# Kernel optimization log

Measured on AMD Instinct MI355X. Metric: run time of the kernel, lower is better.

The kernel has to match this reference:

```python
import jax, jax.numpy as jnp
import numpy as np
import math

B, H, S, D = 4, 16, 2048, 128

def setup_inputs() -> dict:
    key = jax.random.key(0)
    kq, kk, kv = jax.random.split(key, 3)
    Q = jax.random.normal(kq, (B, H, S, D), dtype=jnp.float32)
    K = jax.random.normal(kk, (B, H, S, D), dtype=jnp.float32)
    V = jax.random.normal(kv, (B, H, S, D), dtype=jnp.float32)
    return {"Q": Q, "K": K, "V": V}

def reference(Q, K, V):
    # scores: [B, H, S, S]
    scale = 1.0 / math.sqrt(Q.shape[-1])
    scores = jnp.einsum('bhqd,bhkd->bhqk', Q, K) * scale
    attn = jax.nn.softmax(scores, axis=-1)
    return jnp.einsum('bhqk,bhkd->bhqd', attn, V)
```

## Files before the change

### kernel.cpp

```cpp
#include <hip/hip_runtime.h>
#include <stdint.h>

#define BATCH 4
#define HEADS 16
#define SEQ 2048
#define DIM 128

constexpr int QBLK  = 128;
constexpr int KVB   = 64;
constexpr int NKT   = SEQ / KVB;
constexpr int TILEB = KVB * DIM * 2;
constexpr int NBH   = BATCH * HEADS;

constexpr int K0OFF = 0;
constexpr int K1OFF = 16384;
constexpr int V0OFF = 32768;
constexpr int V1OFF = 49152;

typedef __bf16 bf16x8 __attribute__((ext_vector_type(8)));
typedef float  f32x4  __attribute__((ext_vector_type(4)));
typedef float  f32x16 __attribute__((ext_vector_type(16)));
typedef unsigned int uint32;

typedef const __attribute__((address_space(1))) void* gas_t;
typedef __attribute__((address_space(3))) void* las_t;

__device__ __forceinline__ uint32 packbf2(float a, float b) {
  union { __bf16 h[2]; uint32 u; } c;
  c.h[0] = (__bf16)a; c.h[1] = (__bf16)b;
  return c.u;
}

__global__ __launch_bounds__(256)
void prepass(const float* __restrict__ Kg, const float* __restrict__ Vg,
             char* __restrict__ Kws, char* __restrict__ Vws)
{
  __shared__ __bf16 sVt[DIM * 72];
  const int tile = blockIdx.x;
  const int tid  = threadIdx.x;
  const float* Ksrc = Kg + (size_t)tile * KVB * DIM;
  const float* Vsrc = Vg + (size_t)tile * KVB * DIM;
  char* kdst = Kws + (size_t)tile * TILEB;
  char* vdst = Vws + (size_t)tile * TILEB;

#pragma unroll
  for (int c = 0; c < 4; ++c) {
    const int flat8 = (c * 256 + tid) * 8;
    const int kv = flat8 >> 7, d0 = flat8 & 127;
    union { float4 f; float a[4]; } x0, x1;
    x0.f = *(const float4*)(Ksrc + flat8);
    x1.f = *(const float4*)(Ksrc + flat8 + 4);
    bf16x8 kx;
#pragma unroll
    for (int j = 0; j < 4; ++j) { kx[j] = (__bf16)x0.a[j]; kx[4 + j] = (__bf16)x1.a[j]; }
    *(bf16x8*)(kdst + kv * 256 + ((2 * d0) ^ ((kv & 15) << 4))) = kx;

    union { float4 f; float a[4]; } v0, v1;
    v0.f = *(const float4*)(Vsrc + flat8);
    v1.f = *(const float4*)(Vsrc + flat8 + 4);
#pragma unroll
    for (int j = 0; j < 8; ++j) {
      const int d = d0 + j;
      const float vv = (j < 4) ? v0.a[j] : v1.a[j - 4];
      sVt[d * 72 + (kv ^ (((d >> 3) & 7) << 3))] = (__bf16)vv;
    }
  }
  __syncthreads();
#pragma unroll
  for (int c = 0; c < 4; ++c) {
    const int flat8 = (c * 256 + tid) * 8;
    const int d = flat8 >> 6, kv0 = flat8 & 63;
    bf16x8 row = *(const bf16x8*)(&sVt[d * 72 + (kv0 ^ (((d >> 3) & 7) << 3))]);
    *(bf16x8*)(vdst + (d & 63) * 256 +
               ((((d >> 6) << 7) | (2 * kv0)) ^ (((d & 63) & 15) << 4))) = row;
  }
}


#define QK_BODY(KOFF)                                                            \
  {                                                                              \
    s0 = (f32x16)0.0f; s1 = (f32x16)0.0f;                                        \
    __builtin_amdgcn_s_setprio(1);                                               \
    _Pragma("unroll")                                                            \
    for (int k = 0; k < 8; ++k) {                                                \
      bf16x8 kf0 = *(const bf16x8*)(smem + (KOFF) + akv[k]);                     \
      bf16x8 kf1 = *(const bf16x8*)(smem + (KOFF) + 8192 + akv[k]);              \
      s0 = __builtin_amdgcn_mfma_f32_32x32x16_bf16(kf0, qf[k], s0, 0, 0, 0);     \
      s1 = __builtin_amdgcn_mfma_f32_32x32x16_bf16(kf1, qf[k], s1, 0, 0, 0);     \
    }                                                                            \
    __builtin_amdgcn_s_setprio(0);                                               \
  }

#define PV_BODY(VOFF, PB)                                                        \
  {                                                                              \
    __builtin_amdgcn_s_setprio(1);                                               \
    _Pragma("unroll")                                                            \
    for (int td = 0; td < 4; ++td) {                                             \
      _Pragma("unroll")                                                          \
      for (int k = 0; k < 4; ++k) {                                              \
        const int ab = (td >> 1) ? avh[k] : avv[k];                              \
        bf16x8 vf = *(const bf16x8*)(smem + (VOFF) + ab + (td & 1) * 8192);      \
        oacc[td] = __builtin_amdgcn_mfma_f32_32x32x16_bf16(vf, PB[k], oacc[td], 0, 0, 0); \
      }                                                                          \
    }                                                                            \
    __builtin_amdgcn_s_setprio(0);                                               \
  }

#define EXP_BODY(PB)                                                             \
  {                                                                              \
    uint32 pk[2][8];                                                             \
    float rs = 0.f;                                                              \
    _Pragma("unroll")                                                            \
    for (int i = 0; i < 8; ++i) {                                                \
      float a0 = __builtin_amdgcn_exp2f(s0[2*i]);                                \
      float a1 = __builtin_amdgcn_exp2f(s0[2*i+1]);                              \
      float b0 = __builtin_amdgcn_exp2f(s1[2*i]);                                \
      float b1 = __builtin_amdgcn_exp2f(s1[2*i+1]);                              \
      rs += (a0 + a1) + (b0 + b1);                                               \
      pk[0][i] = packbf2(a0, a1);                                                \
      pk[1][i] = packbf2(b0, b1);                                                \
    }                                                                            \
    lrp += rs;                                                                   \
    _Pragma("unroll")                                                            \
    for (int k4 = 0; k4 < 4; ++k4) {                                             \
      const int T = k4 >> 1, a4 = (k4 & 1) * 4;                                  \
      auto r0 = __builtin_amdgcn_permlane32_swap((int)pk[T][a4+0], (int)pk[T][a4+2], false, false); \
      auto r1 = __builtin_amdgcn_permlane32_swap((int)pk[T][a4+1], (int)pk[T][a4+3], false, false); \
      union { uint32 u[4]; bf16x8 v; } w;                                        \
      w.u[0] = (uint32)r0[0]; w.u[1] = (uint32)r1[0];                            \
      w.u[2] = (uint32)r0[1]; w.u[3] = (uint32)r1[1];                            \
      PB[k4] = w.v;                                                              \
    }                                                                            \
  }

#define STAGE_K(DST, kt)                                                         \
  do {                                                                           \
    const char* p_ = Kt + (size_t)(kt) * TILEB;                                  \
    _Pragma("unroll")                                                            \
    for (int c_ = 0; c_ < 4; ++c_) {                                             \
      const int od_ = c_ * 4096 + wid * 1024;                                    \
      __builtin_amdgcn_global_load_lds((gas_t)(p_ + od_ + lane * 16),            \
                                       (las_t)(smem + (DST) + od_), 16, 0, 0);   \
    }                                                                            \
  } while (0)

#define STAGE_V(DST, kt)                                                         \
  do {                                                                           \
    const char* p_ = Vt + (size_t)(kt) * TILEB;                                  \
    _Pragma("unroll")                                                            \
    for (int c_ = 0; c_ < 4; ++c_) {                                             \
      const int od_ = c_ * 4096 + wid * 1024;                                    \
      __builtin_amdgcn_global_load_lds((gas_t)(p_ + od_ + lane * 16),            \
                                       (las_t)(smem + (DST) + od_), 16, 0, 0);   \
    }                                                                            \
  } while (0)

__global__ __launch_bounds__(256, 2)
void attn_fwd(const float* __restrict__ Qg, float* __restrict__ Og,
              const char* __restrict__ Kws, const char* __restrict__ Vws)
{
  __shared__ __align__(16) char smem[65536];

  const int tid  = threadIdx.x;
  const int lane = tid & 63;
  const int wid  = tid >> 6;
  const int l    = lane & 31;
  const int hi   = lane >> 5;

  const int bid = blockIdx.x;
  const int swz = ((bid & 7) << 7) + (bid >> 3);
  const int bh  = swz >> 4;
  const int qb  = swz & 15;

  const float* Qb = Qg + (size_t)bh * SEQ * DIM;
  float*       Ob = Og + (size_t)bh * SEQ * DIM;
  const char*  Kt = Kws + (size_t)bh * NKT * TILEB;
  const char*  Vt = Vws + (size_t)bh * NKT * TILEB;

  const int q0 = qb * QBLK + wid * 32;

  int akv[8], avv[4], avh[4];
#pragma unroll
  for (int k = 0; k < 8; ++k)
    akv[k] = l * 256 + ((k * 32 + hi * 16) ^ ((l & 15) << 4));
#pragma unroll
  for (int k = 0; k < 4; ++k) {
    avv[k] = l * 256 + ((k * 32 + hi * 16) ^ ((l & 15) << 4));
    avh[k] = avv[k] ^ 128;
  }

  STAGE_K(K0OFF, 0);

  const float qscale = 0.08838834764831845f * 1.4426950408889634f;
  bf16x8 qf[8];
  {
    const float* qrow = Qb + (size_t)(q0 + l) * DIM;
#pragma unroll
    for (int k = 0; k < 8; ++k) {
      const int d0 = k * 16 + hi * 8;
      union { float4 f; float a[4]; } x0, x1;
      x0.f = *(const float4*)(qrow + d0);
      x1.f = *(const float4*)(qrow + d0 + 4);
      bf16x8 f;
#pragma unroll
      for (int j = 0; j < 4; ++j) {
        f[j]     = (__bf16)(x0.a[j] * qscale);
        f[4 + j] = (__bf16)(x1.a[j] * qscale);
      }
      qf[k] = f;
    }
  }

  float lrp = 0.f;
  f32x16 s0, s1;
  bf16x8 pbA[4], pbB[4];
  f32x16 oacc[4];
#pragma unroll
  for (int t = 0; t < 4; ++t) oacc[t] = (f32x16)0.0f;

  __syncthreads();

  STAGE_K(K1OFF, 1);
  STAGE_V(V0OFF, 0);
  QK_BODY(K0OFF);
  EXP_BODY(pbA);
  __syncthreads();

#pragma unroll 1
  for (int t = 1; t <= NKT - 3; t += 2) {
    STAGE_K(K0OFF, t + 1);
    STAGE_V(V1OFF, t);
    QK_BODY(K1OFF);
    PV_BODY(V0OFF, pbA);
    EXP_BODY(pbB);
    __syncthreads();

    STAGE_K(K1OFF, t + 2);
    STAGE_V(V0OFF, t + 1);
    QK_BODY(K0OFF);
    PV_BODY(V1OFF, pbB);
    EXP_BODY(pbA);
    __syncthreads();
  }

  STAGE_V(V1OFF, NKT - 1);
  QK_BODY(K1OFF);
  PV_BODY(V0OFF, pbA);
  EXP_BODY(pbB);
  __syncthreads();
  PV_BODY(V1OFF, pbB);

  const float lrow = lrp + __shfl_xor(lrp, 32, 64);
  const float inv = 1.0f / lrow;
  float* sO = (float*)smem;
  __syncthreads();
#pragma unroll
  for (int td = 0; td < 4; ++td)
#pragma unroll
    for (int rq = 0; rq < 4; ++rq) {
      const int d = td * 32 + rq * 8 + hi * 4;
      f32x4 o;
      o[0] = oacc[td][rq * 4 + 0] * inv;
      o[1] = oacc[td][rq * 4 + 1] * inv;
      o[2] = oacc[td][rq * 4 + 2] * inv;
      o[3] = oacc[td][rq * 4 + 3] * inv;
      *(f32x4*)(&sO[(wid * 32 + l) * 128 + (d ^ (l << 2))]) = o;
    }
  __syncthreads();
#pragma unroll
  for (int c = 0; c < 16; ++c) {
    const int flat4 = (c * 256 + tid) * 4;
    const int q = flat4 >> 7, d0 = flat4 & 127;
    f32x4 o = *(const f32x4*)(&sO[q * 128 + (d0 ^ ((q & 31) << 2))]);
    *(f32x4*)(Ob + (size_t)(qb * QBLK + q) * DIM + d0) = o;
  }
}

extern "C" void kernel_launch(void* const* d_in, const int* in_sizes, int n_in,
                              void* d_out, int out_size, void* d_ws, size_t ws_size,
                              hipStream_t stream) {
  const float* Q = (const float*)d_in[0];
  const float* K = (const float*)d_in[1];
  const float* V = (const float*)d_in[2];
  float* O = (float*)d_out;
  char* Kws = (char*)d_ws;
  char* Vws = Kws + (size_t)NBH * NKT * TILEB;
  prepass<<<NBH * NKT, 256, 0, stream>>>(K, V, Kws, Vws);
  attn_fwd<<<NBH * 16, 256, 0, stream>>>(Q, O, Kws, Vws);
}
```

Before: 188.5 us.

## Triple-buffer K tiles and replace syncthreads with partial vmcnt waits

Adds a third K buffer in LDS (80KB total) so K is prefetched two tiles ahead while V stays double-buffered, and rewrites the main loop as a six-phase unrolled rotation. Full __syncthreads (which drain all outstanding loads) are replaced by s_waitcnt vmcnt(4) plus a raw barrier, letting the next tile's loads stay in flight across the barrier. V address bases are precomputed per buffer. The larger LDS footprint may reduce residency below the two blocks per CU requested, and the hand-tuned vmcnt counts must match load ordering exactly.

```diff
diff --git a/kernel.cpp b/kernel.cpp
--- a/kernel.cpp
+++ b/kernel.cpp
@@ -14,8 +14,9 @@
 
 constexpr int K0OFF = 0;
 constexpr int K1OFF = 16384;
-constexpr int V0OFF = 32768;
-constexpr int V1OFF = 49152;
+constexpr int K2OFF = 32768;
+constexpr int V0OFF = 49152;
+constexpr int V1OFF = 65536;
 
 typedef __bf16 bf16x8 __attribute__((ext_vector_type(8)));
 typedef float  f32x4  __attribute__((ext_vector_type(4)));
@@ -91,15 +92,15 @@
     __builtin_amdgcn_s_setprio(0);                                               \
   }
 
-#define PV_BODY(VOFF, PB)                                                        \
+#define PV_BODY(PAVV, PAVH, PB)                                                  \
   {                                                                              \
     __builtin_amdgcn_s_setprio(1);                                               \
     _Pragma("unroll")                                                            \
     for (int td = 0; td < 4; ++td) {                                             \
       _Pragma("unroll")                                                          \
       for (int k = 0; k < 4; ++k) {                                              \
-        const int ab = (td >> 1) ? avh[k] : avv[k];                              \
-        bf16x8 vf = *(const bf16x8*)(smem + (VOFF) + ab + (td & 1) * 8192);      \
+        const int ab = (td >> 1) ? PAVH[k] : PAVV[k];                            \
+        bf16x8 vf = *(const bf16x8*)(smem + ab + (td & 1) * 8192);               \
         oacc[td] = __builtin_amdgcn_mfma_f32_32x32x16_bf16(vf, PB[k], oacc[td], 0, 0, 0); \
       }                                                                          \
     }                                                                            \
@@ -155,11 +156,22 @@
     }                                                                            \
   } while (0)
 
+#define PHASE(T, KROFF, KWOFF, PAVV, PAVH, VWOFF, PBc, PBp, DO_K, VMN)           \
+  {                                                                              \
+    STAGE_V(VWOFF, (T));                                                         \
+    if (DO_K) STAGE_K(KWOFF, (T) + 2);                                           \
+    QK_BODY(KROFF);                                                              \
+    PV_BODY(PAVV, PAVH, PBp);                                                    \
+    EXP_BODY(PBc);                                                               \
+    asm volatile("s_waitcnt vmcnt(" #VMN ")" ::: "memory");                      \
+    __builtin_amdgcn_s_barrier();                                                \
+  }
+
 __global__ __launch_bounds__(256, 2)
 void attn_fwd(const float* __restrict__ Qg, float* __restrict__ Og,
               const char* __restrict__ Kws, const char* __restrict__ Vws)
 {
-  __shared__ __align__(16) char smem[65536];
+  __shared__ __align__(16) char smem[81920];
 
   const int tid  = threadIdx.x;
   const int lane = tid & 63;
@@ -179,17 +191,16 @@
 
   const int q0 = qb * QBLK + wid * 32;
 
-  int akv[8], avv[4], avh[4];
+  int akv[8], avv0[4], avh0[4], avv1[4], avh1[4];
 #pragma unroll
   for (int k = 0; k < 8; ++k)
     akv[k] = l * 256 + ((k * 32 + hi * 16) ^ ((l & 15) << 4));
 #pragma unroll
   for (int k = 0; k < 4; ++k) {
-    avv[k] = l * 256 + ((k * 32 + hi * 16) ^ ((l & 15) << 4));
-    avh[k] = avv[k] ^ 128;
-  }
-
-  STAGE_K(K0OFF, 0);
+    const int rel = l * 256 + ((k * 32 + hi * 16) ^ ((l & 15) << 4));
+    avv0[k] = V0OFF + rel;  avh0[k] = avv0[k] ^ 128;
+    avv1[k] = V1OFF + rel;  avh1[k] = avv1[k] ^ 128;
+  }
 
   const float qscale = 0.08838834764831845f * 1.4426950408889634f;
   bf16x8 qf[8];
@@ -218,42 +229,41 @@
 #pragma unroll
   for (int t = 0; t < 4; ++t) oacc[t] = (f32x16)0.0f;
 
-  __syncthreads();
-
+  STAGE_K(K0OFF, 0);
   STAGE_K(K1OFF, 1);
-  STAGE_V(V0OFF, 0);
-  QK_BODY(K0OFF);
-  EXP_BODY(pbA);
-  __syncthreads();
+  asm volatile("s_waitcnt vmcnt(4)" ::: "memory");
+  __builtin_amdgcn_s_barrier();
+
+  {
+    STAGE_V(V0OFF, 0);
+    STAGE_K(K2OFF, 2);
+    QK_BODY(K0OFF);
+    EXP_BODY(pbA);
+    asm volatile("s_waitcnt vmcnt(4)" ::: "memory");
+    __builtin_amdgcn_s_barrier();
+  }
 
 #pragma unroll 1
-  for (int t = 1; t <= NKT - 3; t += 2) {
-    STAGE_K(K0OFF, t + 1);
-    STAGE_V(V1OFF, t);
-    QK_BODY(K1OFF);
-    PV_BODY(V0OFF, pbA);
-    EXP_BODY(pbB);
-    __syncthreads();
-
-    STAGE_K(K1OFF, t + 2);
-    STAGE_V(V0OFF, t + 1);
-    QK_BODY(K0OFF);
-    PV_BODY(V1OFF, pbB);
-    EXP_BODY(pbA);
-    __syncthreads();
-  }
-
-  STAGE_V(V1OFF, NKT - 1);
-  QK_BODY(K1OFF);
-  PV_BODY(V0OFF, pbA);
-  EXP_BODY(pbB);
-  __syncthreads();
-  PV_BODY(V1OFF, pbB);
+  for (int b = 1; b <= 19; b += 6) {
+    PHASE(b + 0, K1OFF, K0OFF, avv0, avh0, V1OFF, pbB, pbA, 1, 4)
+    PHASE(b + 1, K2OFF, K1OFF, avv1, avh1, V0OFF, pbA, pbB, 1, 4)
+    PHASE(b + 2, K0OFF, K2OFF, avv0, avh0, V1OFF, pbB, pbA, 1, 4)
+    PHASE(b + 3, K1OFF, K0OFF, avv1, avh1, V0OFF, pbA, pbB, 1, 4)
+    PHASE(b + 4, K2OFF, K1OFF, avv0, avh0, V1OFF, pbB, pbA, 1, 4)
+    PHASE(b + 5, K0OFF, K2OFF, avv1, avh1, V0OFF, pbA, pbB, 1, 4)
+  }
+  PHASE(25, K1OFF, K0OFF, avv0, avh0, V1OFF, pbB, pbA, 1, 4)
+  PHASE(26, K2OFF, K1OFF, avv1, avh1, V0OFF, pbA, pbB, 1, 4)
+  PHASE(27, K0OFF, K2OFF, avv0, avh0, V1OFF, pbB, pbA, 1, 4)
+  PHASE(28, K1OFF, K0OFF, avv1, avh1, V0OFF, pbA, pbB, 1, 4)
+  PHASE(29, K2OFF, K1OFF, avv0, avh0, V1OFF, pbB, pbA, 1, 4)
+  PHASE(30, K0OFF, K2OFF, avv1, avh1, V0OFF, pbA, pbB, 0, 0)
+  PHASE(31, K1OFF, K0OFF, avv0, avh0, V1OFF, pbB, pbA, 0, 0)
+  PV_BODY(avv1, avh1, pbB);
 
   const float lrow = lrp + __shfl_xor(lrp, 32, 64);
   const float inv = 1.0f / lrow;
   float* sO = (float*)smem;
-  __syncthreads();
 #pragma unroll
   for (int td = 0; td < 4; ++td)
 #pragma unroll
```

After: 597.5 us. +217.0%, slower.

## Single-buffer K tile to cut LDS to 48KB and allow three blocks per CU

Applied to the files above, without the earlier changes.

Drops the second K buffer so shared memory shrinks from 64KB to 48KB, and raises launch bounds to 3 blocks per CU. The pipeline is reordered so QK reads the single K buffer, then a barrier, then the next K/V tiles are staged while exp and softmax run. The output epilogue is split into two 64-column passes so it fits the smaller LDS. This trades K prefetch overlap and adds barriers per iteration in exchange for higher occupancy, and the tighter register budget at 3 blocks may cause spills.

```diff
diff --git a/kernel.cpp b/kernel.cpp
--- a/kernel.cpp
+++ b/kernel.cpp
@@ -13,9 +13,8 @@
 constexpr int NBH   = BATCH * HEADS;
 
 constexpr int K0OFF = 0;
-constexpr int K1OFF = 16384;
-constexpr int V0OFF = 32768;
-constexpr int V1OFF = 49152;
+constexpr int V0OFF = 16384;
+constexpr int V1OFF = 32768;
 
 typedef __bf16 bf16x8 __attribute__((ext_vector_type(8)));
 typedef float  f32x4  __attribute__((ext_vector_type(4)));
@@ -77,14 +76,14 @@
 }
 
 
-#define QK_BODY(KOFF)                                                            \
+#define QK_BODY()                                                                \
   {                                                                              \
     s0 = (f32x16)0.0f; s1 = (f32x16)0.0f;                                        \
     __builtin_amdgcn_s_setprio(1);                                               \
     _Pragma("unroll")                                                            \
     for (int k = 0; k < 8; ++k) {                                                \
-      bf16x8 kf0 = *(const bf16x8*)(smem + (KOFF) + akv[k]);                     \
-      bf16x8 kf1 = *(const bf16x8*)(smem + (KOFF) + 8192 + akv[k]);              \
+      bf16x8 kf0 = *(const bf16x8*)(smem + akv[k]);                              \
+      bf16x8 kf1 = *(const bf16x8*)(smem + 8192 + akv[k]);                       \
       s0 = __builtin_amdgcn_mfma_f32_32x32x16_bf16(kf0, qf[k], s0, 0, 0, 0);     \
       s1 = __builtin_amdgcn_mfma_f32_32x32x16_bf16(kf1, qf[k], s1, 0, 0, 0);     \
     }                                                                            \
@@ -133,9 +132,20 @@
     }                                                                            \
   }
 
-#define STAGE_K(DST, kt)                                                         \
+#define STAGE_K(kt)                                                              \
   do {                                                                           \
     const char* p_ = Kt + (size_t)(kt) * TILEB;                                  \
+    _Pragma("unroll")                                                            \
+    for (int c_ = 0; c_ < 4; ++c_) {                                             \
+      const int od_ = c_ * 4096 + wid * 1024;                                    \
+      __builtin_amdgcn_global_load_lds((gas_t)(p_ + od_ + lane * 16),            \
+                                       (las_t)(smem + od_), 16, 0, 0);           \
+    }                                                                            \
+  } while (0)
+
+#define STAGE_V(DST, kt)                                                         \
+  do {                                                                           \
+    const char* p_ = Vt + (size_t)(kt) * TILEB;                                  \
     _Pragma("unroll")                                                            \
     for (int c_ = 0; c_ < 4; ++c_) {                                             \
       const int od_ = c_ * 4096 + wid * 1024;                                    \
@@ -144,22 +154,11 @@
     }                                                                            \
   } while (0)
 
-#define STAGE_V(DST, kt)                                                         \
-  do {                                                                           \
-    const char* p_ = Vt + (size_t)(kt) * TILEB;                                  \
-    _Pragma("unroll")                                                            \
-    for (int c_ = 0; c_ < 4; ++c_) {                                             \
-      const int od_ = c_ * 4096 + wid * 1024;                                    \
-      __builtin_amdgcn_global_load_lds((gas_t)(p_ + od_ + lane * 16),            \
-                                       (las_t)(smem + (DST) + od_), 16, 0, 0);   \
-    }                                                                            \
-  } while (0)
-
-__global__ __launch_bounds__(256, 2)
+__global__ __launch_bounds__(256, 3)
 void attn_fwd(const float* __restrict__ Qg, float* __restrict__ Og,
               const char* __restrict__ Kws, const char* __restrict__ Vws)
 {
-  __shared__ __align__(16) char smem[65536];
+  __shared__ __align__(16) char smem[49152];
 
   const int tid  = threadIdx.x;
   const int lane = tid & 63;
@@ -189,7 +188,7 @@
     avh[k] = avv[k] ^ 128;
   }
 
-  STAGE_K(K0OFF, 0);
+  STAGE_K(0);
 
   const float qscale = 0.08838834764831845f * 1.4426950408889634f;
   bf16x8 qf[8];
@@ -219,33 +218,36 @@
   for (int t = 0; t < 4; ++t) oacc[t] = (f32x16)0.0f;
 
   __syncthreads();
-
-  STAGE_K(K1OFF, 1);
+  QK_BODY();
+  __syncthreads();
+  STAGE_K(1);
   STAGE_V(V0OFF, 0);
-  QK_BODY(K0OFF);
   EXP_BODY(pbA);
-  __syncthreads();
 
 #pragma unroll 1
-  for (int t = 1; t <= NKT - 3; t += 2) {
-    STAGE_K(K0OFF, t + 1);
-    STAGE_V(V1OFF, t);
-    QK_BODY(K1OFF);
+  for (int b = 1; b <= 29; b += 2) {
+    __syncthreads();
+    QK_BODY();
     PV_BODY(V0OFF, pbA);
+    __syncthreads();
+    STAGE_K(b + 1);
+    STAGE_V(V1OFF, b);
     EXP_BODY(pbB);
-    __syncthreads();
-
-    STAGE_K(K1OFF, t + 2);
-    STAGE_V(V0OFF, t + 1);
-    QK_BODY(K0OFF);
+
+    __syncthreads();
+    QK_BODY();
     PV_BODY(V1OFF, pbB);
+    __syncthreads();
+    STAGE_K(b + 2);
+    STAGE_V(V0OFF, b + 1);
     EXP_BODY(pbA);
-    __syncthreads();
-  }
-
-  STAGE_V(V1OFF, NKT - 1);
-  QK_BODY(K1OFF);
+  }
+
+  __syncthreads();
+  QK_BODY();
   PV_BODY(V0OFF, pbA);
+  __syncthreads();
+  STAGE_V(V1OFF, 31);
   EXP_BODY(pbB);
   __syncthreads();
   PV_BODY(V1OFF, pbB);
@@ -253,26 +255,31 @@
   const float lrow = lrp + __shfl_xor(lrp, 32, 64);
   const float inv = 1.0f / lrow;
   float* sO = (float*)smem;
-  __syncthreads();
-#pragma unroll
-  for (int td = 0; td < 4; ++td)
-#pragma unroll
-    for (int rq = 0; rq < 4; ++rq) {
-      const int d = td * 32 + rq * 8 + hi * 4;
-      f32x4 o;
-      o[0] = oacc[td][rq * 4 + 0] * inv;
-      o[1] = oacc[td][rq * 4 + 1] * inv;
-      o[2] = oacc[td][rq * 4 + 2] * inv;
-      o[3] = oacc[td][rq * 4 + 3] * inv;
-      *(f32x4*)(&sO[(wid * 32 + l) * 128 + (d ^ (l << 2))]) = o;
-    }
-  __syncthreads();
-#pragma unroll
-  for (int c = 0; c < 16; ++c) {
-    const int flat4 = (c * 256 + tid) * 4;
-    const int q = flat4 >> 7, d0 = flat4 & 127;
-    f32x4 o = *(const f32x4*)(&sO[q * 128 + (d0 ^ ((q & 31) << 2))]);
-    *(f32x4*)(Ob + (size_t)(qb * QBLK + q) * DIM + d0) = o;
+#pragma unroll
+  for (int pass = 0; pass < 2; ++pass) {
+    if (pass) __syncthreads();
+#pragma unroll
+    for (int td2 = 0; td2 < 2; ++td2) {
+      const int td = pass * 2 + td2;
+#pragma unroll
+      for (int rq = 0; rq < 4; ++rq) {
+        const int dp = td2 * 32 + rq * 8 + hi * 4;
+        f32x4 o;
+        o[0] = oacc[td][rq * 4 + 0] * inv;
+        o[1] = oacc[td][rq * 4 + 1] * inv;
+        o[2] = oacc[td][rq * 4 + 2] * inv;
+        o[3] = oacc[td][rq * 4 + 3] * inv;
+        *(f32x4*)(&sO[(wid * 32 + l) * 64 + (dp ^ ((l & 15) << 2))]) = o;
+      }
+    }
+    __syncthreads();
+#pragma unroll
+    for (int c = 0; c < 8; ++c) {
+      const int flat4 = (c * 256 + tid) * 4;
+      const int q = flat4 >> 6, dp0 = flat4 & 63;
+      f32x4 o = *(const f32x4*)(&sO[q * 64 + (dp0 ^ ((q & 15) << 2))]);
+      *(f32x4*)(Ob + (size_t)(qb * QBLK + q) * DIM + pass * 64 + dp0) = o;
+    }
   }
 }
 
```

Result: slower. 386.2 us (+104.9%).
